# Kernel tuning notes

Measured on AMD Instinct MI355X. Metric: run time of the kernel, lower is better.

## Reference

```python
import jax, jax.numpy as jnp
import numpy as np

B, T, D = 2, 2048, 2048
H, G = 16, 4          # query heads, kv groups (GQA)
DK = D // H           # 128
THETA = 10000.0


def _rope(x, pos):
    # x: (B, h, T, dk); half-split rotary embedding
    dk = x.shape[-1]
    inv_freq = 1.0 / (THETA ** (jnp.arange(0, dk // 2, dtype=jnp.float32) * 2.0 / dk))
    ang = pos.astype(jnp.float32)[:, None] * inv_freq[None, :]   # (T, dk/2)
    cos, sin = jnp.cos(ang), jnp.sin(ang)                        # (T, dk/2)
    x1, x2 = x[..., : dk // 2], x[..., dk // 2 :]
    return jnp.concatenate([x1 * cos - x2 * sin, x2 * cos + x1 * sin], axis=-1)


def setup_inputs() -> dict:
    key = jax.random.key(0)
    ks = jax.random.split(key, 5)
    scale = D ** -0.5
    x = jax.random.normal(ks[0], (B, T, D), jnp.float32)
    Wq = jax.random.normal(ks[1], (D, H * DK), jnp.float32) * scale
    Wk = jax.random.normal(ks[2], (D, G * DK), jnp.float32) * scale
    Wv = jax.random.normal(ks[3], (D, G * DK), jnp.float32) * scale
    Wo = jax.random.normal(ks[4], (D, D), jnp.float32) * scale
    mask = jnp.tril(jnp.ones((T, T), dtype=bool))   # causal mask, True = attend
    pos = jnp.arange(T, dtype=jnp.int32)
    return {"x": x, "Wq": Wq, "Wk": Wk, "Wv": Wv, "Wo": Wo, "mask": mask, "pos": pos}


def reference(x, Wq, Wk, Wv, Wo, mask, pos):
    b, t, d = x.shape
    # projections (bias-free linears)
    q = (x @ Wq).reshape(b, t, H, DK).transpose(0, 2, 1, 3)   # (b, h, t, dk)
    k = (x @ Wk).reshape(b, t, G, DK).transpose(0, 2, 1, 3)   # (b, g, t, dk)
    v = (x @ Wv).reshape(b, t, G, DK).transpose(0, 2, 1, 3)
    # RoPE on q and k (module applies rope_q(q,q) and rope_k(k,k))
    q = _rope(q, pos)
    k = _rope(k, pos)
    # GQA: repeat_interleave kv heads to match query heads
    rf = H // G
    k = jnp.repeat(k, rf, axis=1)   # (b, h, t, dk)
    v = jnp.repeat(v, rf, axis=1)
    # scores + causal mask + softmax
    att = jnp.einsum('bhtd,bhTd->bhtT', q, k) / np.float32(np.sqrt(DK))
    att = jnp.where(mask[None, None, :, :], att, -jnp.inf)
    att = jax.nn.softmax(att, axis=-1)
    y = jnp.einsum('bhtT,bhTd->bhtd', att, v)
    y = y.transpose(0, 2, 1, 3).reshape(b, t, d)
    return y @ Wo
```

## Files before the change

kernel.cpp:

```cpp
#include <hip/hip_runtime.h>
#include <cstdint>
#include <cmath>


#define GLOBAL_AS __attribute__((address_space(1)))
#define LDS_AS __attribute__((address_space(3)))

typedef __bf16 bf16x8 __attribute__((ext_vector_type(8)));
typedef __bf16 bf16x4 __attribute__((ext_vector_type(4)));
typedef float f32x4 __attribute__((ext_vector_type(4)));

constexpr int Tn = 2048;

__device__ __forceinline__ f32x4 mfma_bf16(bf16x8 a, bf16x8 b, f32x4 c) {
  return __builtin_amdgcn_mfma_f32_16x16x32_bf16(a, b, c, 0, 0, 0);
}

__global__ __launch_bounds__(256) void convert_f32_bf16(const float* __restrict__ src,
                                                        __bf16* __restrict__ dst,
                                                        size_t n4) {
  const size_t i = (size_t)blockIdx.x * 256 + threadIdx.x;
  if (i >= n4) return;
  const f32x4 v = ((const f32x4*)src)[i];
  bf16x4 o;
#pragma unroll
  for (int k = 0; k < 4; ++k) o[k] = (__bf16)v[k];
  ((bf16x4*)dst)[i] = o;
}

__global__ __launch_bounds__(256) void transpose_f32_bf16(const float* __restrict__ src,
                                                          __bf16* __restrict__ dst,
                                                          int K, int N) {
  __shared__ __bf16 tile[32][33];
  const int n0 = blockIdx.x * 32, k0 = blockIdx.y * 32;
  const int tx = threadIdx.x, ty = threadIdx.y;
#pragma unroll
  for (int i = 0; i < 32; i += 8)
    tile[ty + i][tx] = (__bf16)src[(size_t)(k0 + ty + i) * N + n0 + tx];
  __syncthreads();
#pragma unroll
  for (int i = 0; i < 32; i += 8)
    dst[(size_t)(n0 + ty + i) * K + k0 + tx] = tile[tx][ty + i];
}

__global__ __launch_bounds__(256) void transpose_v(const __bf16* __restrict__ qkv,
                                                   __bf16* __restrict__ vtg) {
  __shared__ __bf16 tile[32][33];
  const int bg = blockIdx.z;
  const int b = bg >> 2, g = bg & 3;
  const int key0 = blockIdx.x * 32, d0 = blockIdx.y * 32;
  const int tx = threadIdx.x, ty = threadIdx.y;
  const __bf16* src = qkv + (size_t)b * Tn * 3072 + 2560 + g * 128;
  __bf16* dst = vtg + (size_t)bg * 128 * Tn;
#pragma unroll
  for (int i = 0; i < 32; i += 8)
    tile[ty + i][tx] = src[(size_t)(key0 + ty + i) * 3072 + d0 + tx];
  __syncthreads();
#pragma unroll
  for (int i = 0; i < 32; i += 8)
    dst[(size_t)(d0 + ty + i) * Tn + key0 + tx] = tile[tx][ty + i];
}

__global__ __launch_bounds__(256) void gemm_bt(const __bf16* __restrict__ A,
                                               const __bf16* __restrict__ BT,
                                               void* __restrict__ C,
                                               int K, int ldc, int outf32) {
  __shared__ __attribute__((aligned(16))) __bf16 As[128 * 32];
  __shared__ __attribute__((aligned(16))) __bf16 Bs[128 * 32];
  const int tid = threadIdx.x;
  const int wave = tid >> 6, lane = tid & 63;
  const int lr = lane & 15, lq = lane >> 4;
  const int wm = wave >> 1, wn = wave & 1;
  const int m0 = blockIdx.y * 128, n0 = blockIdx.x * 128;

  f32x4 acc[4][4] = {};

  const int srow = tid >> 2;
  const int scol = (tid & 3) * 8;
  const __bf16* ga = A + (size_t)(m0 + srow) * K + scol;
  const __bf16* gb = BT + (size_t)(n0 + srow) * K + scol;

  for (int kt = 0; kt < K; kt += 32) {
    __syncthreads();
#pragma unroll
    for (int it = 0; it < 2; ++it) {
      __builtin_amdgcn_global_load_lds((GLOBAL_AS void*)(ga + (size_t)it * 64 * K + kt),
                                       (LDS_AS void*)(As + it * 2048 + wave * 512), 16, 0, 0);
      __builtin_amdgcn_global_load_lds((GLOBAL_AS void*)(gb + (size_t)it * 64 * K + kt),
                                       (LDS_AS void*)(Bs + it * 2048 + wave * 512), 16, 0, 0);
    }
    __syncthreads();

    bf16x8 af[4], bfv[4];
#pragma unroll
    for (int i = 0; i < 4; ++i)
      af[i] = *(const bf16x8*)(As + (wm * 64 + i * 16 + lr) * 32 + lq * 8);
#pragma unroll
    for (int j = 0; j < 4; ++j)
      bfv[j] = *(const bf16x8*)(Bs + (wn * 64 + j * 16 + lr) * 32 + lq * 8);
#pragma unroll
    for (int i = 0; i < 4; ++i)
#pragma unroll
      for (int j = 0; j < 4; ++j)
        acc[i][j] = mfma_bf16(af[i], bfv[j], acc[i][j]);
  }

#pragma unroll
  for (int i = 0; i < 4; ++i) {
    const int row = m0 + wm * 64 + i * 16 + lq * 4;
#pragma unroll
    for (int j = 0; j < 4; ++j) {
      const int col = n0 + wn * 64 + j * 16 + lr;
#pragma unroll
      for (int r = 0; r < 4; ++r) {
        if (outf32)
          ((float*)C)[(size_t)(row + r) * ldc + col] = acc[i][j][r];
        else
          ((__bf16*)C)[(size_t)(row + r) * ldc + col] = (__bf16)acc[i][j][r];
      }
    }
  }
}

__global__ __launch_bounds__(256) void rope_kernel(__bf16* __restrict__ qkv) {
  const int row = blockIdx.x;
  const int t = row & (Tn - 1);
  for (int p = threadIdx.x; p < 1280; p += 256) {
    const int d = p & 63;
    const int hh = p >> 6;
    const int col = (hh < 16) ? (hh * 128 + d) : (2048 + (hh - 16) * 128 + d);
    const float inv = exp2f((float)d * (-13.287712379549449f / 64.f));
    const float ang = (float)t * inv;
    float sn, cs;
    __sincosf(ang, &sn, &cs);
    __bf16* ptr = qkv + (size_t)row * 3072 + col;
    const float x1 = (float)ptr[0];
    const float x2 = (float)ptr[64];
    ptr[0] = (__bf16)(x1 * cs - x2 * sn);
    ptr[64] = (__bf16)(x2 * cs + x1 * sn);
  }
}

constexpr int KVB = 64;
__global__ __launch_bounds__(512, 4) void flash_attn(const __bf16* __restrict__ qkv,
                                                     const __bf16* __restrict__ vtg,
                                                     __bf16* __restrict__ y) {
  const int b = blockIdx.y >> 4, h = blockIdx.y & 15;
  const int g = h >> 2;
  const int q0 = ((int)gridDim.x - 1 - (int)blockIdx.x) * 128;
  const int tid = threadIdx.x;
  const int wave = tid >> 6, lane = tid & 63;
  const int lr = lane & 15, lq = lane >> 4;

  const __bf16* Qb = qkv + (size_t)b * Tn * 3072 + h * 128;
  const __bf16* Kb = qkv + (size_t)b * Tn * 3072 + 2048 + g * 128;
  const __bf16* Vt = vtg + (size_t)(b * 4 + g) * 128 * Tn;

  __shared__ __attribute__((aligned(16))) __bf16 Ks[2][8192];
  __shared__ __attribute__((aligned(16))) __bf16 Vs[2][8192];
  __shared__ __attribute__((aligned(16))) __bf16 Pl[8][1024];

  const __bf16* ksrc[2];
  const __bf16* vsrc[2];
#pragma unroll
  for (int i = 0; i < 2; ++i) {
    ksrc[i] = Kb + (size_t)((i * 2 + (wave >> 2)) * 16 + lr) * 3072 + (wave & 3) * 32 + lq * 8;
    vsrc[i] = Vt + (size_t)((i * 4 + (wave >> 1)) * 16 + lr) * Tn + (wave & 1) * 32 + lq * 8;
  }

  const int qrow = q0 + wave * 16 + lr;
  bf16x8 qf[4];
#pragma unroll
  for (int f = 0; f < 4; ++f)
    qf[f] = *(const bf16x8*)(Qb + (size_t)qrow * 3072 + f * 32 + lq * 8);

  f32x4 o[8] = {};
  float m_i[4], l_i[4];
#pragma unroll
  for (int r = 0; r < 4; ++r) { m_i[r] = -1e30f; l_i[r] = 0.f; }
  const float kscale = 0.12752909695983215f;

  __bf16* Plw = &Pl[wave][0];
  const int lr7 = lr & 7, lrh = lr >> 3;
  const int pbase = lq * 32 + lr7;

#pragma unroll
  for (int i = 0; i < 2; ++i) {
    __builtin_amdgcn_global_load_lds((GLOBAL_AS void*)ksrc[i],
                                     (LDS_AS void*)(&Ks[0][(i * 512 + wave * 64) * 8]), 16, 0, 0);
    __builtin_amdgcn_global_load_lds((GLOBAL_AS void*)vsrc[i],
                                     (LDS_AS void*)(&Vs[0][(i * 512 + wave * 64) * 8]), 16, 0, 0);
    ksrc[i] += (size_t)KVB * 3072;
    vsrc[i] += KVB;
  }
  __syncthreads();

  const int ktend = q0 + 128;
  int cur = 0;
  for (int kt = 0; kt < ktend; kt += KVB) {
    if (kt + KVB < ktend) {
#pragma unroll
      for (int i = 0; i < 2; ++i) {
        __builtin_amdgcn_global_load_lds(
            (GLOBAL_AS void*)ksrc[i],
            (LDS_AS void*)(&Ks[cur ^ 1][(i * 512 + wave * 64) * 8]), 16, 0, 0);
        __builtin_amdgcn_global_load_lds(
            (GLOBAL_AS void*)vsrc[i],
            (LDS_AS void*)(&Vs[cur ^ 1][(i * 512 + wave * 64) * 8]), 16, 0, 0);
        ksrc[i] += (size_t)KVB * 3072;
        vsrc[i] += KVB;
      }
    }

    const bool active = kt <= q0 + wave * 16 + 15;
    if (active) {
      f32x4 s[4] = {};
      __builtin_amdgcn_s_setprio(1);
#pragma unroll
      for (int sub = 0; sub < 4; ++sub)
#pragma unroll
        for (int f = 0; f < 4; ++f) {
          const bf16x8 kf = *(const bf16x8*)(&Ks[cur][((sub * 4 + f) * 64 + lane) * 8]);
          s[sub] = mfma_bf16(qf[f], kf, s[sub]);
        }
      __builtin_amdgcn_s_setprio(0);

      const bool full = (kt + KVB - 1) <= (q0 + wave * 16);
      float mx[4];
      bool need = false;
#pragma unroll
      for (int r = 0; r < 4; ++r) {
        if (full) {
#pragma unroll
          for (int c = 0; c < 4; ++c) s[c][r] = s[c][r] * kscale;
        } else {
          const int q = q0 + wave * 16 + lq * 4 + r;
#pragma unroll
          for (int c = 0; c < 4; ++c)
            s[c][r] = (kt + c * 16 + lr <= q) ? s[c][r] * kscale : -1e30f;
        }
        float m = fmaxf(fmaxf(s[0][r], s[1][r]), fmaxf(s[2][r], s[3][r]));
        m = fmaxf(m, __shfl_xor(m, 1));
        m = fmaxf(m, __shfl_xor(m, 2));
        m = fmaxf(m, __shfl_xor(m, 4));
        m = fmaxf(m, __shfl_xor(m, 8));
        mx[r] = m;
        need = need || (m > m_i[r] + 8.f);
      }
      if (__any(need)) {
#pragma unroll
        for (int r = 0; r < 4; ++r) {
          const float mnew = fmaxf(m_i[r], mx[r]);
          const float alpha = __builtin_amdgcn_exp2f(m_i[r] - mnew);
          m_i[r] = mnew;
          l_i[r] *= alpha;
#pragma unroll
          for (int n = 0; n < 8; ++n) o[n][r] *= alpha;
        }
      }
#pragma unroll
      for (int r = 0; r < 4; ++r) {
#pragma unroll
        for (int c = 0; c < 4; ++c) {
          const float pv = __builtin_amdgcn_exp2f(s[c][r] - m_i[r]);
          l_i[r] += pv;
          Plw[(c >> 1) * 512 + ((c & 1) * 2 + lrh) * 128 + pbase + r * 8] = (__bf16)pv;
        }
      }

      __threadfence_block();

      const bf16x8 pa0 = *(const bf16x8*)(Plw + lane * 8);
      const bf16x8 pa1 = *(const bf16x8*)(Plw + (64 + lane) * 8);
      __builtin_amdgcn_s_setprio(1);
#pragma unroll
      for (int n = 0; n < 8; ++n) {
        const bf16x8 v0 = *(const bf16x8*)(&Vs[cur][((n * 2 + 0) * 64 + lane) * 8]);
        const bf16x8 v1 = *(const bf16x8*)(&Vs[cur][((n * 2 + 1) * 64 + lane) * 8]);
        o[n] = mfma_bf16(pa0, v0, o[n]);
        o[n] = mfma_bf16(pa1, v1, o[n]);
      }
      __builtin_amdgcn_s_setprio(0);
    }

    __syncthreads();
    cur ^= 1;
  }

#pragma unroll
  for (int r = 0; r < 4; ++r) {
    float l = l_i[r];
    l += __shfl_xor(l, 1);
    l += __shfl_xor(l, 2);
    l += __shfl_xor(l, 4);
    l += __shfl_xor(l, 8);
    const float inv = 1.0f / l;
    const int q = q0 + wave * 16 + lq * 4 + r;
#pragma unroll
    for (int n = 0; n < 8; ++n)
      y[(size_t)(b * Tn + q) * 2048 + h * 128 + n * 16 + lr] = (__bf16)(o[n][r] * inv);
  }
}

extern "C" void kernel_launch(void* const* d_in, const int* in_sizes, int n_in,
                              void* d_out, int out_size, void* d_ws, size_t ws_size,
                              hipStream_t stream) {
  (void)in_sizes; (void)n_in; (void)out_size; (void)ws_size;
  const float* x  = (const float*)d_in[0];
  const float* Wq = (const float*)d_in[1];
  const float* Wk = (const float*)d_in[2];
  const float* Wv = (const float*)d_in[3];
  const float* Wo = (const float*)d_in[4];
  float* out = (float*)d_out;

  __bf16* xb  = (__bf16*)d_ws;
  __bf16* y   = xb;
  __bf16* WT  = xb + (size_t)4096 * 2048;
  __bf16* WoT = WT;
  __bf16* VtG = WT + (size_t)2048 * 2048;
  __bf16* qkv = WT + (size_t)3072 * 2048;

  convert_f32_bf16<<<(4096 * 2048 / 4 + 255) / 256, 256, 0, stream>>>(x, xb, 4096 * 2048 / 4);
  dim3 tb(32, 8);
  transpose_f32_bf16<<<dim3(64, 64), tb, 0, stream>>>(Wq, WT, 2048, 2048);
  transpose_f32_bf16<<<dim3(16, 64), tb, 0, stream>>>(Wk, WT + (size_t)2048 * 2048, 2048, 512);
  transpose_f32_bf16<<<dim3(16, 64), tb, 0, stream>>>(Wv, WT + (size_t)2560 * 2048, 2048, 512);

  gemm_bt<<<dim3(3072 / 128, 4096 / 128), 256, 0, stream>>>(xb, WT, qkv, 2048, 3072, 0);
  rope_kernel<<<4096, 256, 0, stream>>>(qkv);

  transpose_v<<<dim3(Tn / 32, 4, 8), tb, 0, stream>>>(qkv, VtG);
  transpose_f32_bf16<<<dim3(64, 64), tb, 0, stream>>>(Wo, WoT, 2048, 2048);

  flash_attn<<<dim3(Tn / 128, 2 * 16), 512, 0, stream>>>(qkv, VtG, y);
  gemm_bt<<<dim3(2048 / 128, 4096 / 128), 256, 0, stream>>>(y, WoT, out, 2048, 2048, 1);
}
```

Measured before the change: 388.9 us.

## Rewrite flash attention with 32x32 MFMA and register-resident P fragments

Switches the attention kernel from 16x16x32 MFMA with 8 waves of 16 query rows to 32x32x16 MFMA with 4 waves of 32 query rows each. S is computed transposed (K as A operand) so each lane owns one query row, which removes the cross-lane max/sum shuffles except one xor-32. The softmax probabilities are packed to bf16 and exchanged between lane halves with shuffles instead of being staged through LDS, removing the per-wave P scratch buffer and its fence. Block size drops to 256 threads with a higher per-thread register budget, which trades occupancy for larger MFMA tiles and fewer LDS round-trips.

```diff
diff --git a/kernel.cpp b/kernel.cpp
--- a/kernel.cpp
+++ b/kernel.cpp
@@ -9,11 +9,21 @@
 typedef __bf16 bf16x8 __attribute__((ext_vector_type(8)));
 typedef __bf16 bf16x4 __attribute__((ext_vector_type(4)));
 typedef float f32x4 __attribute__((ext_vector_type(4)));
+typedef float f32x16 __attribute__((ext_vector_type(16)));
 
 constexpr int Tn = 2048;
 
 __device__ __forceinline__ f32x4 mfma_bf16(bf16x8 a, bf16x8 b, f32x4 c) {
   return __builtin_amdgcn_mfma_f32_16x16x32_bf16(a, b, c, 0, 0, 0);
+}
+__device__ __forceinline__ f32x16 mfma32(bf16x8 a, bf16x8 b, f32x16 c) {
+  return __builtin_amdgcn_mfma_f32_32x32x16_bf16(a, b, c, 0, 0, 0);
+}
+__device__ __forceinline__ uint32_t pack_bf16(float a, float b) {
+  union { __bf16 h[2]; uint32_t u; } c;
+  c.h[0] = (__bf16)a;
+  c.h[1] = (__bf16)b;
+  return c.u;
 }
 
 __global__ __launch_bounds__(256) void convert_f32_bf16(const float* __restrict__ src,
@@ -142,7 +152,7 @@
 }
 
 constexpr int KVB = 64;
-__global__ __launch_bounds__(512, 4) void flash_attn(const __bf16* __restrict__ qkv,
+__global__ __launch_bounds__(256, 2) void flash_attn(const __bf16* __restrict__ qkv,
                                                      const __bf16* __restrict__ vtg,
                                                      __bf16* __restrict__ y) {
   const int b = blockIdx.y >> 4, h = blockIdx.y & 15;
@@ -150,7 +160,7 @@
   const int q0 = ((int)gridDim.x - 1 - (int)blockIdx.x) * 128;
   const int tid = threadIdx.x;
   const int wave = tid >> 6, lane = tid & 63;
-  const int lr = lane & 15, lq = lane >> 4;
+  const int l31 = lane & 31, hi = lane >> 5;
 
   const __bf16* Qb = qkv + (size_t)b * Tn * 3072 + h * 128;
   const __bf16* Kb = qkv + (size_t)b * Tn * 3072 + 2048 + g * 128;
@@ -158,38 +168,31 @@
 
   __shared__ __attribute__((aligned(16))) __bf16 Ks[2][8192];
   __shared__ __attribute__((aligned(16))) __bf16 Vs[2][8192];
-  __shared__ __attribute__((aligned(16))) __bf16 Pl[8][1024];
-
-  const __bf16* ksrc[2];
-  const __bf16* vsrc[2];
-#pragma unroll
-  for (int i = 0; i < 2; ++i) {
-    ksrc[i] = Kb + (size_t)((i * 2 + (wave >> 2)) * 16 + lr) * 3072 + (wave & 3) * 32 + lq * 8;
-    vsrc[i] = Vt + (size_t)((i * 4 + (wave >> 1)) * 16 + lr) * Tn + (wave & 1) * 32 + lq * 8;
-  }
-
-  const int qrow = q0 + wave * 16 + lr;
-  bf16x8 qf[4];
-#pragma unroll
-  for (int f = 0; f < 4; ++f)
-    qf[f] = *(const bf16x8*)(Qb + (size_t)qrow * 3072 + f * 32 + lq * 8);
-
-  f32x4 o[8] = {};
-  float m_i[4], l_i[4];
-#pragma unroll
-  for (int r = 0; r < 4; ++r) { m_i[r] = -1e30f; l_i[r] = 0.f; }
+
+  const __bf16* ksrc[4];
+  const __bf16* vsrc[4];
+#pragma unroll
+  for (int i = 0; i < 4; ++i) {
+    ksrc[i] = Kb + (size_t)((i >> 1) * 32 + l31) * 3072 + ((i * 4 + wave) & 7) * 16 + hi * 8;
+    vsrc[i] = Vt + (size_t)(i * 32 + l31) * Tn + wave * 16 + hi * 8;
+  }
+
+  const int qg = q0 + wave * 32 + l31;
+  bf16x8 qf[8];
+#pragma unroll
+  for (int s = 0; s < 8; ++s)
+    qf[s] = *(const bf16x8*)(Qb + (size_t)qg * 3072 + s * 16 + hi * 8);
+
+  f32x16 o[4] = {};
+  float m_i = -1e30f, l_i = 0.f;
   const float kscale = 0.12752909695983215f;
 
-  __bf16* Plw = &Pl[wave][0];
-  const int lr7 = lr & 7, lrh = lr >> 3;
-  const int pbase = lq * 32 + lr7;
-
-#pragma unroll
-  for (int i = 0; i < 2; ++i) {
+#pragma unroll
+  for (int i = 0; i < 4; ++i) {
     __builtin_amdgcn_global_load_lds((GLOBAL_AS void*)ksrc[i],
-                                     (LDS_AS void*)(&Ks[0][(i * 512 + wave * 64) * 8]), 16, 0, 0);
+                                     (LDS_AS void*)(&Ks[0][(i * 256 + wave * 64) * 8]), 16, 0, 0);
     __builtin_amdgcn_global_load_lds((GLOBAL_AS void*)vsrc[i],
-                                     (LDS_AS void*)(&Vs[0][(i * 512 + wave * 64) * 8]), 16, 0, 0);
+                                     (LDS_AS void*)(&Vs[0][(i * 256 + wave * 64) * 8]), 16, 0, 0);
     ksrc[i] += (size_t)KVB * 3072;
     vsrc[i] += KVB;
   }
@@ -200,86 +203,111 @@
   for (int kt = 0; kt < ktend; kt += KVB) {
     if (kt + KVB < ktend) {
 #pragma unroll
-      for (int i = 0; i < 2; ++i) {
+      for (int i = 0; i < 4; ++i) {
         __builtin_amdgcn_global_load_lds(
             (GLOBAL_AS void*)ksrc[i],
-            (LDS_AS void*)(&Ks[cur ^ 1][(i * 512 + wave * 64) * 8]), 16, 0, 0);
+            (LDS_AS void*)(&Ks[cur ^ 1][(i * 256 + wave * 64) * 8]), 16, 0, 0);
         __builtin_amdgcn_global_load_lds(
             (GLOBAL_AS void*)vsrc[i],
-            (LDS_AS void*)(&Vs[cur ^ 1][(i * 512 + wave * 64) * 8]), 16, 0, 0);
+            (LDS_AS void*)(&Vs[cur ^ 1][(i * 256 + wave * 64) * 8]), 16, 0, 0);
         ksrc[i] += (size_t)KVB * 3072;
         vsrc[i] += KVB;
       }
     }
 
-    const bool active = kt <= q0 + wave * 16 + 15;
-    if (active) {
-      f32x4 s[4] = {};
+    if (kt <= q0 + wave * 32 + 31) {
+      f32x16 sa[2] = {};
       __builtin_amdgcn_s_setprio(1);
 #pragma unroll
-      for (int sub = 0; sub < 4; ++sub)
-#pragma unroll
-        for (int f = 0; f < 4; ++f) {
-          const bf16x8 kf = *(const bf16x8*)(&Ks[cur][((sub * 4 + f) * 64 + lane) * 8]);
-          s[sub] = mfma_bf16(qf[f], kf, s[sub]);
+      for (int kb = 0; kb < 2; ++kb)
+#pragma unroll
+        for (int s = 0; s < 8; ++s) {
+          const bf16x8 kf = *(const bf16x8*)(&Ks[cur][((kb * 8 + s) * 64 + lane) * 8]);
+          sa[kb] = mfma32(kf, qf[s], sa[kb]);
         }
       __builtin_amdgcn_s_setprio(0);
 
-      const bool full = (kt + KVB - 1) <= (q0 + wave * 16);
-      float mx[4];
-      bool need = false;
-#pragma unroll
-      for (int r = 0; r < 4; ++r) {
-        if (full) {
-#pragma unroll
-          for (int c = 0; c < 4; ++c) s[c][r] = s[c][r] * kscale;
-        } else {
-          const int q = q0 + wave * 16 + lq * 4 + r;
-#pragma unroll
-          for (int c = 0; c < 4; ++c)
-            s[c][r] = (kt + c * 16 + lr <= q) ? s[c][r] * kscale : -1e30f;
+      const bool full = (kt + KVB - 1) <= (q0 + wave * 32);
+      float mx = -1e30f;
+      if (full) {
+#pragma unroll
+        for (int kb = 0; kb < 2; ++kb)
+#pragma unroll
+          for (int r = 0; r < 16; ++r) {
+            const float v = sa[kb][r] * kscale;
+            sa[kb][r] = v;
+            mx = fmaxf(mx, v);
+          }
+      } else {
+#pragma unroll
+        for (int kb = 0; kb < 2; ++kb)
+#pragma unroll
+          for (int r = 0; r < 16; ++r) {
+            const int key = kt + kb * 32 + (r & 3) + 8 * (r >> 2) + 4 * hi;
+            const float v = (key <= qg) ? sa[kb][r] * kscale : -1e30f;
+            sa[kb][r] = v;
+            mx = fmaxf(mx, v);
+          }
+      }
+      mx = fmaxf(mx, __shfl_xor(mx, 32));
+      if (__any(mx > m_i + 8.f)) {
+        const float mnew = fmaxf(m_i, mx);
+        const float alpha = __builtin_amdgcn_exp2f(m_i - mnew);
+        m_i = mnew;
+        l_i *= alpha;
+#pragma unroll
+        for (int db = 0; db < 4; ++db)
+#pragma unroll
+          for (int r = 0; r < 16; ++r) o[db][r] *= alpha;
+      }
+      float ls = 0.f;
+#pragma unroll
+      for (int kb = 0; kb < 2; ++kb)
+#pragma unroll
+        for (int r = 0; r < 16; ++r) {
+          const float pv = __builtin_amdgcn_exp2f(sa[kb][r] - m_i);
+          sa[kb][r] = pv;
+          ls += pv;
         }
-        float m = fmaxf(fmaxf(s[0][r], s[1][r]), fmaxf(s[2][r], s[3][r]));
-        m = fmaxf(m, __shfl_xor(m, 1));
-        m = fmaxf(m, __shfl_xor(m, 2));
-        m = fmaxf(m, __shfl_xor(m, 4));
-        m = fmaxf(m, __shfl_xor(m, 8));
-        mx[r] = m;
-        need = need || (m > m_i[r] + 8.f);
-      }
-      if (__any(need)) {
-#pragma unroll
-        for (int r = 0; r < 4; ++r) {
-          const float mnew = fmaxf(m_i[r], mx[r]);
-          const float alpha = __builtin_amdgcn_exp2f(m_i[r] - mnew);
-          m_i[r] = mnew;
-          l_i[r] *= alpha;
-#pragma unroll
-          for (int n = 0; n < 8; ++n) o[n][r] *= alpha;
+      l_i += ls;
+
+      uint32_t P[2][8], X[2][8];
+#pragma unroll
+      for (int kb = 0; kb < 2; ++kb)
+#pragma unroll
+        for (int gg = 0; gg < 8; ++gg)
+          P[kb][gg] = pack_bf16(sa[kb][2 * gg], sa[kb][2 * gg + 1]);
+#pragma unroll
+      for (int kb = 0; kb < 2; ++kb)
+#pragma unroll
+        for (int gg = 0; gg < 8; ++gg)
+          X[kb][gg] = (uint32_t)__shfl_xor((int)P[kb][gg], 32);
+
+      union FU { uint32_t u[4]; bf16x8 v; };
+      bf16x8 pf[4];
+#pragma unroll
+      for (int kb = 0; kb < 2; ++kb) {
+        FU f0, f1;
+        f0.u[0] = hi ? X[kb][2] : P[kb][0];
+        f0.u[1] = hi ? X[kb][3] : P[kb][1];
+        f0.u[2] = hi ? P[kb][2] : X[kb][0];
+        f0.u[3] = hi ? P[kb][3] : X[kb][1];
+        f1.u[0] = hi ? X[kb][6] : P[kb][4];
+        f1.u[1] = hi ? X[kb][7] : P[kb][5];
+        f1.u[2] = hi ? P[kb][6] : X[kb][4];
+        f1.u[3] = hi ? P[kb][7] : X[kb][5];
+        pf[kb * 2 + 0] = f0.v;
+        pf[kb * 2 + 1] = f1.v;
+      }
+
+      __builtin_amdgcn_s_setprio(1);
+#pragma unroll
+      for (int db = 0; db < 4; ++db)
+#pragma unroll
+        for (int s = 0; s < 4; ++s) {
+          const bf16x8 vf = *(const bf16x8*)(&Vs[cur][((db * 4 + s) * 64 + lane) * 8]);
+          o[db] = mfma32(vf, pf[s], o[db]);
         }
-      }
-#pragma unroll
-      for (int r = 0; r < 4; ++r) {
-#pragma unroll
-        for (int c = 0; c < 4; ++c) {
-          const float pv = __builtin_amdgcn_exp2f(s[c][r] - m_i[r]);
-          l_i[r] += pv;
-          Plw[(c >> 1) * 512 + ((c & 1) * 2 + lrh) * 128 + pbase + r * 8] = (__bf16)pv;
-        }
-      }
-
-      __threadfence_block();
-
-      const bf16x8 pa0 = *(const bf16x8*)(Plw + lane * 8);
-      const bf16x8 pa1 = *(const bf16x8*)(Plw + (64 + lane) * 8);
-      __builtin_amdgcn_s_setprio(1);
-#pragma unroll
-      for (int n = 0; n < 8; ++n) {
-        const bf16x8 v0 = *(const bf16x8*)(&Vs[cur][((n * 2 + 0) * 64 + lane) * 8]);
-        const bf16x8 v1 = *(const bf16x8*)(&Vs[cur][((n * 2 + 1) * 64 + lane) * 8]);
-        o[n] = mfma_bf16(pa0, v0, o[n]);
-        o[n] = mfma_bf16(pa1, v1, o[n]);
-      }
       __builtin_amdgcn_s_setprio(0);
     }
 
@@ -287,18 +315,19 @@
     cur ^= 1;
   }
 
-#pragma unroll
-  for (int r = 0; r < 4; ++r) {
-    float l = l_i[r];
-    l += __shfl_xor(l, 1);
-    l += __shfl_xor(l, 2);
-    l += __shfl_xor(l, 4);
-    l += __shfl_xor(l, 8);
-    const float inv = 1.0f / l;
-    const int q = q0 + wave * 16 + lq * 4 + r;
-#pragma unroll
-    for (int n = 0; n < 8; ++n)
-      y[(size_t)(b * Tn + q) * 2048 + h * 128 + n * 16 + lr] = (__bf16)(o[n][r] * inv);
+  {
+    const float lt = l_i + __shfl_xor(l_i, 32);
+    const float inv = 1.0f / lt;
+    __bf16* yrow = y + (size_t)(b * Tn + qg) * 2048 + h * 128;
+#pragma unroll
+    for (int db = 0; db < 4; ++db)
+#pragma unroll
+      for (int g2 = 0; g2 < 4; ++g2) {
+        bf16x4 ov;
+#pragma unroll
+        for (int j = 0; j < 4; ++j) ov[j] = (__bf16)(o[db][4 * g2 + j] * inv);
+        *(bf16x4*)(yrow + db * 32 + 8 * g2 + 4 * hi) = ov;
+      }
   }
 }
 
@@ -332,6 +361,6 @@
   transpose_v<<<dim3(Tn / 32, 4, 8), tb, 0, stream>>>(qkv, VtG);
   transpose_f32_bf16<<<dim3(64, 64), tb, 0, stream>>>(Wo, WoT, 2048, 2048);
 
-  flash_attn<<<dim3(Tn / 128, 2 * 16), 512, 0, stream>>>(qkv, VtG, y);
+  flash_attn<<<dim3(Tn / 128, 2 * 16), 256, 0, stream>>>(qkv, VtG, y);
   gemm_bt<<<dim3(2048 / 128, 4096 / 128), 256, 0, stream>>>(y, WoT, out, 2048, 2048, 1);
 }
```

After: 369.8 us. 4.9% less time.
